# Optimization experiments

Hardware: AMD Instinct MI355X
Metric: run time of the kernel (lower is better)

## Reference

```python
import jax, jax.numpy as jnp
import numpy as np
from jax import lax

WINDOW_SIZE = 11
SIGMA = 1.5
C1 = 0.01 ** 2
C2 = 0.03 ** 2


def _create_window(window_size, channel):
    xs = np.arange(window_size)
    g = np.exp(-((xs - window_size // 2) ** 2) / (2.0 * SIGMA ** 2))
    g = (g / g.sum()).astype(np.float32)
    w2d = np.outer(g, g)  # [k, k]
    # depthwise kernel in OIHW with feature_group_count=channel: [channel, 1, k, k]
    return jnp.asarray(np.broadcast_to(w2d, (channel, 1, window_size, window_size)).copy())


def _dw_conv(x, window, pad):
    # x: [B, C, H, W], window: [C, 1, k, k]; depthwise conv, SAME-style padding
    c = x.shape[1]
    return lax.conv_general_dilated(
        x, window,
        window_strides=(1, 1),
        padding=[(pad, pad), (pad, pad)],
        dimension_numbers=('NCHW', 'OIHW', 'NCHW'),
        feature_group_count=c,
    )


def setup_inputs() -> dict:
    key = jax.random.key(0)
    k1, k2 = jax.random.split(key)
    img1 = jax.random.uniform(k1, (32, 1, 512, 512), dtype=jnp.float32)
    img2 = jax.random.uniform(k2, (32, 1, 512, 512), dtype=jnp.float32)
    return {"img1": img1, "img2": img2}


def reference(img1, img2):
    channel = img1.shape[1]
    pad = WINDOW_SIZE // 2
    window = _create_window(WINDOW_SIZE, channel)

    mu1 = _dw_conv(img1, window, pad)
    mu2 = _dw_conv(img2, window, pad)
    mu1_sq = mu1 * mu1
    mu2_sq = mu2 * mu2
    mu1_mu2 = mu1 * mu2

    sigma1_sq = _dw_conv(img1 * img1, window, pad) - mu1_sq
    sigma2_sq = _dw_conv(img2 * img2, window, pad) - mu2_sq
    sigma12 = _dw_conv(img1 * img2, window, pad) - mu1_mu2

    ssim_map = ((2.0 * mu1_mu2 + C1) * (2.0 * sigma12 + C2)) / (
        (mu1_sq + mu2_sq + C1) * (sigma1_sq + sigma2_sq + C2))
    return 1.0 - jnp.mean(ssim_map)
```

## Files before the change

### kernel.cpp

```cpp
#include <hip/hip_runtime.h>

typedef _Float16 f16x8 __attribute__((ext_vector_type(8)));
typedef _Float16 f16x4 __attribute__((ext_vector_type(4)));
typedef __fp16 fp16x2 __attribute__((ext_vector_type(2)));
typedef float f32x4 __attribute__((ext_vector_type(4)));

#define IMG 512
#define NB 32
#define OUTC 118
#define OUTR 32
#define GX 5
#define GY 16
#define NBLK (GX*GY*NB)
#define INSTR 48
#define IOFF (128*INSTR)
#define VSTR 136
#define VOFF (16*VSTR)
#define VLEN (5*VOFF + 32)
#define BUF0 (2*IOFF)

#define GW_LIST { 0.0010283804f, 0.0075987583f, 0.0360007700f, 0.1093606900f, \
  0.2130055300f, 0.2660117200f, 0.2130055300f, 0.1093606900f, 0.0360007700f, \
  0.0075987583f, 0.0010283804f }

__global__ __launch_bounds__(256, 3) void ssim_mfma(const float* __restrict__ img1,
                                                    const float* __restrict__ img2,
                                                    float* __restrict__ partials) {
    __shared__ _Float16 smem[BUF0 + VLEN];
    __shared__ float red[4];

    const int tid  = threadIdx.x;
    const int lane = tid & 63;
    const int lm   = lane & 15;
    const int kg   = lane >> 4;
    const int w    = tid >> 6;

    const int d   = (blockIdx.z * GY + blockIdx.y) * GX + blockIdx.x;
    const int wid = (d & 7) * (NBLK / 8) + (d >> 3);
    const int bx  = wid % GX;
    const int t2  = wid / GX;
    const int by  = t2 % GY;
    const int bz  = t2 / GY;

    const float* __restrict__ p1 = img1 + (size_t)bz * (IMG*IMG);
    const float* __restrict__ p2 = img2 + (size_t)bz * (IMG*IMG);
    const int x0 = bx * OUTC;
    const int y0 = by * OUTR;

    union { fp16x2 p[4]; f16x8 v; } wu;
    {
        const float GWc[11] = GW_LIST;
        float gf = 0.f;
#pragma unroll
        for (int k = 0; k < 11; ++k) gf = (lane == k) ? GWc[k] : gf;
        const int gi = __float_as_int(gf);
        float hv[8];
#pragma unroll
        for (int i = 0; i < 8; ++i) {
            const int t = kg*8 + i - lm;
            const int bp = __builtin_amdgcn_ds_bpermute(t * 4, gi);
            hv[i] = ((unsigned)t < 11u) ? __int_as_float(bp) : 0.f;
        }
#pragma unroll
        for (int j = 0; j < 4; ++j)
            wu.p[j] = __builtin_amdgcn_cvt_pkrtz(hv[2*j], hv[2*j+1]);
    }

    {
        const int cl   = lane & 31;
        const int half = lane >> 5;
        const int ci   = w*32 + cl;
        const int gc   = x0 - 5 + ci;
        const bool okc = (gc >= 0) && (gc < IMG);
        const int gcc  = okc ? gc : 0;
        const int slot0 = half * 24;

        union { fp16x2 p2v[12]; f16x8 v[3]; } ua, ub;
#pragma unroll
        for (int pp = 0; pp < 12; ++pp) {
            const int s0 = slot0 + 2*pp;
            const int ar0 = y0 - 5 + s0;
            const int ar1 = ar0 + 1;
            const bool ok0 = okc & (s0   < 42) & (ar0 >= 0) & (ar0 < IMG);
            const bool ok1 = okc & (s0+1 < 42) & (ar1 >= 0) & (ar1 < IMG);
            const int i0 = ok0 ? ar0 : 0, i1 = ok1 ? ar1 : 0;
            float a0 = p1[i0*IMG + gcc], a1 = p1[i1*IMG + gcc];
            float b0 = p2[i0*IMG + gcc], b1 = p2[i1*IMG + gcc];
            a0 = ok0 ? a0 : 0.f;  a1 = ok1 ? a1 : 0.f;
            b0 = ok0 ? b0 : 0.f;  b1 = ok1 ? b1 : 0.f;
            ua.p2v[pp] = __builtin_amdgcn_cvt_pkrtz(a0, a1);
            ub.p2v[pp] = __builtin_amdgcn_cvt_pkrtz(b0, b1);
        }
        _Float16* dst = &smem[ci*INSTR + slot0];
#pragma unroll
        for (int m = 0; m < 3; ++m) {
            *(f16x8*)(dst + 8*m)        = ua.v[m];
            *(f16x8*)(dst + IOFF + 8*m) = ub.v[m];
        }
    }

    const f32x4 zc = {0.f, 0.f, 0.f, 0.f};

    f16x4 pk[2][2][5];
#pragma unroll
    for (int s = 0; s < 2; ++s) {
#pragma unroll
        for (int q = 0; q < 2; ++q) {
            const int cb = 2*w + q;
            const _Float16* colp = &smem[(cb*16 + lm)*INSTR + s*16 + kg*8];
            const f16x8 xf = *(const f16x8*)colp;
            const f16x8 yf = *(const f16x8*)(colp + IOFF);
            const f16x8 fr[5] = { xf, yf, xf*xf, yf*yf, xf*yf };
#pragma unroll
            for (int f = 0; f < 5; ++f) {
                const f32x4 dd = __builtin_amdgcn_mfma_f32_16x16x32_f16(fr[f], wu.v, zc, 0, 0, 0);
                union { fp16x2 p[2]; f16x4 v4; } c;
                c.p[0] = __builtin_amdgcn_cvt_pkrtz(dd[0], dd[1]);
                c.p[1] = __builtin_amdgcn_cvt_pkrtz(dd[2], dd[3]);
                pk[s][q][f] = c.v4;
            }
        }
    }

    {
        _Float16* b = &smem[BUF0 + lm*VSTR + 2*w*16 + kg*4];
#pragma unroll
        for (int q = 0; q < 2; ++q)
#pragma unroll
            for (int f = 0; f < 5; ++f)
                *(f16x4*)(b + f*VOFF + q*16) = pk[0][q][f];

        f16x8 z = {};
        if (tid < 80) {
            const int f = tid / 16, r = tid % 16;
            *(f16x8*)&smem[BUF0 + f*VOFF + r*VSTR + 128] = z;
        } else if (tid < 84) {
            *(f16x8*)&smem[BUF0 + 5*VOFF + (tid-80)*8] = z;
        }
    }
    __syncthreads();

    {
        _Float16* b = &smem[lm*VSTR + 2*w*16 + kg*4];
#pragma unroll
        for (int q = 0; q < 2; ++q)
#pragma unroll
            for (int f = 0; f < 5; ++f)
                *(f16x4*)(b + f*VOFF + q*16) = pk[1][q][f];
    }

    float local = 0.f;
    auto stage_h = [&](int base) {
#pragma unroll
        for (int q = 0; q < 2; ++q) {
            const int xx = 2*w + q;
            const _Float16* vp = &smem[base + lm*VSTR + xx*16 + kg*8];
            f32x4 dd[5];
#pragma unroll
            for (int f = 0; f < 5; ++f) {
                const f16x8 a = *(const f16x8*)(vp + f*VOFF);
                dd[f] = __builtin_amdgcn_mfma_f32_16x16x32_f16(a, wu.v, zc, 0, 0, 0);
            }
            const int X = xx*16 + lm;
            const bool valid = (X < OUTC) & (x0 + X < IMG);
            float s4 = 0.f;
#pragma unroll
            for (int j = 0; j < 4; ++j) {
                const float mu1 = dd[0][j], mu2 = dd[1][j];
                const float m11 = mu1*mu1, m22 = mu2*mu2, m12 = mu1*mu2;
                const float s1 = dd[2][j] - m11, s2 = dd[3][j] - m22, sx = dd[4][j] - m12;
                const float num = (2.f*m12 + 1e-4f) * (2.f*sx + 9e-4f);
                const float den = (m11 + m22 + 1e-4f) * (s1 + s2 + 9e-4f);
                s4 += num * __builtin_amdgcn_rcpf(den);
            }
            local += valid ? s4 : 0.f;
        }
    };

    stage_h(BUF0);
    __syncthreads();
    stage_h(0);

#pragma unroll
    for (int off = 32; off > 0; off >>= 1)
        local += __shfl_down(local, off, 64);
    if (lane == 0) red[w] = local;
    __syncthreads();
    if (tid == 0) {
        partials[(size_t)wid] = red[0] + red[1] + red[2] + red[3];
    }
}

__global__ __launch_bounds__(256) void ssim_finalize(const float* __restrict__ partials,
                                                     float* __restrict__ out) {
    __shared__ double red[4];
    double s = 0.0;
    for (int i = threadIdx.x; i < NBLK/4; i += 256) {
        const float4 v = reinterpret_cast<const float4*>(partials)[i];
        s += (double)v.x + (double)v.y + (double)v.z + (double)v.w;
    }
#pragma unroll
    for (int off = 32; off > 0; off >>= 1)
        s += __shfl_down(s, off, 64);
    if ((threadIdx.x & 63) == 0) red[threadIdx.x >> 6] = s;
    __syncthreads();
    if (threadIdx.x == 0) {
        double tot = red[0] + red[1] + red[2] + red[3];
        out[0] = (float)(1.0 - tot / (32.0 * 512.0 * 512.0));
    }
}

extern "C" void kernel_launch(void* const* d_in, const int* in_sizes, int n_in,
                              void* d_out, int out_size, void* d_ws, size_t ws_size,
                              hipStream_t stream) {
    const float* img1 = (const float*)d_in[0];
    const float* img2 = (const float*)d_in[1];
    float* out = (float*)d_out;
    float* partials = (float*)d_ws;

    dim3 grid(GX, GY, NB);
    ssim_mfma<<<grid, 256, 0, stream>>>(img1, img2, partials);
    ssim_finalize<<<1, 256, 0, stream>>>(partials, out);
}
```

Measured before the change: 25.81 us.

## Widen column tile to 128 outputs with extra halo column block on wave 3

Changes the output tile from 118 to 128 columns so the grid has 4 column blocks instead of 5, removing the partially wasted fifth block and the per-column validity masking. The 10 extra halo columns are loaded by half of wave 3 and their vertical pass is done by wave 3 as a ninth 16-column block. This cuts total blocks and redundant halo loads, at the cost of load imbalance on wave 3 and larger shared-memory strides.

```diff
diff --git a/kernel.cpp b/kernel.cpp
--- a/kernel.cpp
+++ b/kernel.cpp
@@ -7,14 +7,14 @@
 
 #define IMG 512
 #define NB 32
-#define OUTC 118
-#define OUTR 32
-#define GX 5
+#define OUTC 128
+#define GX 4
 #define GY 16
 #define NBLK (GX*GY*NB)
 #define INSTR 48
-#define IOFF (128*INSTR)
-#define VSTR 136
+#define ICOL 144
+#define IOFF (ICOL*INSTR)
+#define VSTR 152
 #define VOFF (16*VSTR)
 #define VLEN (5*VOFF + 32)
 #define BUF0 (2*IOFF)
@@ -45,7 +45,7 @@
     const float* __restrict__ p1 = img1 + (size_t)bz * (IMG*IMG);
     const float* __restrict__ p2 = img2 + (size_t)bz * (IMG*IMG);
     const int x0 = bx * OUTC;
-    const int y0 = by * OUTR;
+    const int y0 = by * 32;
 
     union { fp16x2 p[4]; f16x8 v; } wu;
     {
@@ -66,15 +66,11 @@
             wu.p[j] = __builtin_amdgcn_cvt_pkrtz(hv[2*j], hv[2*j+1]);
     }
 
-    {
-        const int cl   = lane & 31;
-        const int half = lane >> 5;
-        const int ci   = w*32 + cl;
-        const int gc   = x0 - 5 + ci;
-        const bool okc = (gc >= 0) && (gc < IMG);
-        const int gcc  = okc ? gc : 0;
+    auto stage_cols = [&](int ci, int half) {
+        const int gc = x0 - 5 + ci;
+        const bool okc = (gc >= 0) && (gc < IMG) && (ci < 138);
+        const int gcc = okc ? gc : 0;
         const int slot0 = half * 24;
-
         union { fp16x2 p2v[12]; f16x8 v[3]; } ua, ub;
 #pragma unroll
         for (int pp = 0; pp < 12; ++pp) {
@@ -97,29 +93,40 @@
             *(f16x8*)(dst + 8*m)        = ua.v[m];
             *(f16x8*)(dst + IOFF + 8*m) = ub.v[m];
         }
-    }
+    };
+
+    stage_cols(w*32 + (lane & 31), lane >> 5);
+    if (w == 3 && lane < 32)
+        stage_cols(128 + (lane & 15), (lane >> 4) & 1);
 
     const f32x4 zc = {0.f, 0.f, 0.f, 0.f};
 
+    auto vcomp = [&](int cb, int s, f16x4 out[5]) {
+        const _Float16* colp = &smem[(cb*16 + lm)*INSTR + s*16 + kg*8];
+        const f16x8 xf = *(const f16x8*)colp;
+        const f16x8 yf = *(const f16x8*)(colp + IOFF);
+        const f16x8 fr[5] = { xf, yf, xf*xf, yf*yf, xf*yf };
+#pragma unroll
+        for (int f = 0; f < 5; ++f) {
+            const f32x4 dd = __builtin_amdgcn_mfma_f32_16x16x32_f16(fr[f], wu.v, zc, 0, 0, 0);
+            union { fp16x2 p[2]; f16x4 v4; } c;
+            c.p[0] = __builtin_amdgcn_cvt_pkrtz(dd[0], dd[1]);
+            c.p[1] = __builtin_amdgcn_cvt_pkrtz(dd[2], dd[3]);
+            out[f] = c.v4;
+        }
+    };
+
     f16x4 pk[2][2][5];
-#pragma unroll
-    for (int s = 0; s < 2; ++s) {
-#pragma unroll
-        for (int q = 0; q < 2; ++q) {
-            const int cb = 2*w + q;
-            const _Float16* colp = &smem[(cb*16 + lm)*INSTR + s*16 + kg*8];
-            const f16x8 xf = *(const f16x8*)colp;
-            const f16x8 yf = *(const f16x8*)(colp + IOFF);
-            const f16x8 fr[5] = { xf, yf, xf*xf, yf*yf, xf*yf };
-#pragma unroll
-            for (int f = 0; f < 5; ++f) {
-                const f32x4 dd = __builtin_amdgcn_mfma_f32_16x16x32_f16(fr[f], wu.v, zc, 0, 0, 0);
-                union { fp16x2 p[2]; f16x4 v4; } c;
-                c.p[0] = __builtin_amdgcn_cvt_pkrtz(dd[0], dd[1]);
-                c.p[1] = __builtin_amdgcn_cvt_pkrtz(dd[2], dd[3]);
-                pk[s][q][f] = c.v4;
-            }
-        }
+    f16x4 pk8[2][5];
+#pragma unroll
+    for (int s = 0; s < 2; ++s)
+#pragma unroll
+        for (int q = 0; q < 2; ++q)
+            vcomp(2*w + q, s, pk[s][q]);
+    if (w == 3) {
+#pragma unroll
+        for (int s = 0; s < 2; ++s)
+            vcomp(8, s, pk8[s]);
     }
 
     {
@@ -129,13 +136,11 @@
 #pragma unroll
             for (int f = 0; f < 5; ++f)
                 *(f16x4*)(b + f*VOFF + q*16) = pk[0][q][f];
-
-        f16x8 z = {};
-        if (tid < 80) {
-            const int f = tid / 16, r = tid % 16;
-            *(f16x8*)&smem[BUF0 + f*VOFF + r*VSTR + 128] = z;
-        } else if (tid < 84) {
-            *(f16x8*)&smem[BUF0 + 5*VOFF + (tid-80)*8] = z;
+        if (w == 3) {
+            _Float16* b8 = &smem[BUF0 + lm*VSTR + 128 + kg*4];
+#pragma unroll
+            for (int f = 0; f < 5; ++f)
+                *(f16x4*)(b8 + f*VOFF) = pk8[0][f];
         }
     }
     __syncthreads();
@@ -147,6 +152,12 @@
 #pragma unroll
             for (int f = 0; f < 5; ++f)
                 *(f16x4*)(b + f*VOFF + q*16) = pk[1][q][f];
+        if (w == 3) {
+            _Float16* b8 = &smem[lm*VSTR + 128 + kg*4];
+#pragma unroll
+            for (int f = 0; f < 5; ++f)
+                *(f16x4*)(b8 + f*VOFF) = pk8[1][f];
+        }
     }
 
     float local = 0.f;
@@ -161,9 +172,6 @@
                 const f16x8 a = *(const f16x8*)(vp + f*VOFF);
                 dd[f] = __builtin_amdgcn_mfma_f32_16x16x32_f16(a, wu.v, zc, 0, 0, 0);
             }
-            const int X = xx*16 + lm;
-            const bool valid = (X < OUTC) & (x0 + X < IMG);
-            float s4 = 0.f;
 #pragma unroll
             for (int j = 0; j < 4; ++j) {
                 const float mu1 = dd[0][j], mu2 = dd[1][j];
@@ -171,9 +179,8 @@
                 const float s1 = dd[2][j] - m11, s2 = dd[3][j] - m22, sx = dd[4][j] - m12;
                 const float num = (2.f*m12 + 1e-4f) * (2.f*sx + 9e-4f);
                 const float den = (m11 + m22 + 1e-4f) * (s1 + s2 + 9e-4f);
-                s4 += num * __builtin_amdgcn_rcpf(den);
+                local += num * __builtin_amdgcn_rcpf(den);
             }
-            local += valid ? s4 : 0.f;
         }
     };
 
```

Result: slower. 27.29 us (+5.7%).
